# Performance work log

Measured on AMD Instinct MI355X. Metric: run time of the kernel, lower is better.

The kernel has to match this reference:

```python
import jax, jax.numpy as jnp
import numpy as np
import math

B, H, N, DH = 4, 8, 1024, 128
DPT = 4  # point feature dim (<=4 branch: squared-distance map only)

def setup_inputs() -> dict:
    key = jax.random.key(0)
    ks = jax.random.split(key, 10)
    q   = jax.random.normal(ks[0], (B, H, N, DH), jnp.float32)
    k   = jax.random.normal(ks[1], (B, H, N, DH), jnp.float32)
    v   = jax.random.normal(ks[2], (B, H, N, DH), jnp.float32)
    c   = jax.random.normal(ks[3], (B, H, N, 1), jnp.float32)
    d_q = jax.random.normal(ks[4], (B, N, DPT), jnp.float32)
    d_k = jax.random.normal(ks[5], (B, N, DPT), jnp.float32)
    # LazyLinear(1 -> nhead): per-head scalar weight + bias
    w_w = jax.random.normal(ks[6], (H,), jnp.float32) * 0.1
    b_w = jax.random.normal(ks[7], (H,), jnp.float32) * 0.1
    w_b = jax.random.normal(ks[8], (H,), jnp.float32) * 0.1
    b_b = jax.random.normal(ks[9], (H,), jnp.float32) * 0.1
    return {"q": q, "k": k, "v": v, "c": c, "d_q": d_q, "d_k": d_k,
            "w_w": w_w, "b_w": b_w, "w_b": w_b, "b_b": b_b}

def reference(q, k, v, c, d_q, d_k, w_w, b_w, w_b, b_b):
    dh = q.shape[-1]
    # pairwise squared distances on first 3 coords (torch: under no_grad)
    dq3 = d_q[:, :, :3]
    dk3 = d_k[:, :, :3]
    dist = jax.lax.stop_gradient(
        jnp.sum(dq3 ** 2, -1)[:, :, None]
        + jnp.sum(dk3 ** 2, -1)[:, None, :]
        - 2.0 * jnp.einsum('bnd,bmd->bnm', dq3, dk3))  # [B,N,M]
    db = dist[:, None, :, :]  # [B,1,N,M]
    wbc = lambda p: p[None, :, None, None]  # [1,H,1,1]
    # distmap_w = softplus(-(w*dist + b)); distmap_b = w*dist + b (identity acts)
    distmap_w = jax.nn.softplus(-(db * wbc(w_w) + wbc(b_w)))  # [B,H,N,M]
    distmap_b = db * wbc(w_b) + wbc(b_b)                      # [B,H,N,M]
    # scaled dot-product scores per head
    scores = jnp.einsum('bhnd,bhmd->bhnm', q, k) / math.sqrt(dh)
    scores = jax.nn.relu(scores * distmap_w + distmap_b)
    detr = (jnp.sum(scores, -1, keepdims=True)
            + jnp.sum(jax.nn.softplus(c), 2, keepdims=True) + 1e-9)
    scores = scores / detr
    out = jnp.einsum('bhnm,bhmd->bhnd', scores, v)
    return out, scores
```

## Files before the change

### kernel.cpp

```cpp
#include <hip/hip_runtime.h>


typedef __attribute__((ext_vector_type(8))) short short8;
typedef __attribute__((ext_vector_type(4))) float f32x4;

#define OUT_ELEMS 4194304ull
#define WS_K      0ull
#define WS_VT     8388608ull
#define WS_INVD   16777216ull
#define WS_CS     16908288ull

__device__ __forceinline__ unsigned short f2bf(float f) {
    unsigned u = __builtin_bit_cast(unsigned, f);
    u += 0x7FFFu + ((u >> 16) & 1u);
    return (unsigned short)(u >> 16);
}
__device__ __forceinline__ float softplus(float x) {
    return fmaxf(x, 0.f) + __logf(1.f + __expf(-fabsf(x)));
}

__global__ __launch_bounds__(256) void prep_k(const float* __restrict__ k, unsigned short* __restrict__ wsK) {
    int t = blockIdx.x * 256 + threadIdx.x;
    for (int u = t; u < 524288; u += 131072) {
        float4 a = reinterpret_cast<const float4*>(k)[u * 2];
        float4 b = reinterpret_cast<const float4*>(k)[u * 2 + 1];
        short8 o;
        o[0]=(short)f2bf(a.x); o[1]=(short)f2bf(a.y); o[2]=(short)f2bf(a.z); o[3]=(short)f2bf(a.w);
        o[4]=(short)f2bf(b.x); o[5]=(short)f2bf(b.y); o[6]=(short)f2bf(b.z); o[7]=(short)f2bf(b.w);
        reinterpret_cast<short8*>(wsK)[u] = o;
    }
}

__global__ __launch_bounds__(256) void prep_v(const float* __restrict__ v, unsigned short* __restrict__ wsVt) {
    __shared__ unsigned short sT[64 * 132];
    const int bh = blockIdx.x >> 4, m0 = (blockIdx.x & 15) * 64;
    const int tid = threadIdx.x;
    const float* src = v + ((size_t)bh * 1024 + m0) * 128;
    for (int i = tid; i < 2048; i += 256) {
        int row = i >> 5, c4 = i & 31;
        float4 t = reinterpret_cast<const float4*>(src)[i];
        unsigned long long pk = (unsigned long long)f2bf(t.x)
                              | ((unsigned long long)f2bf(t.y) << 16)
                              | ((unsigned long long)f2bf(t.z) << 32)
                              | ((unsigned long long)f2bf(t.w) << 48);
        *reinterpret_cast<unsigned long long*>(&sT[row * 132 + c4 * 4]) = pk;
    }
    __syncthreads();
    for (int u = tid; u < 2048; u += 256) {
        int dh = u >> 4, ms = u & 15;
        unsigned long long pk = (unsigned long long)sT[(ms*4+0)*132 + dh]
                              | ((unsigned long long)sT[(ms*4+1)*132 + dh] << 16)
                              | ((unsigned long long)sT[(ms*4+2)*132 + dh] << 32)
                              | ((unsigned long long)sT[(ms*4+3)*132 + dh] << 48);
        *reinterpret_cast<unsigned long long*>(&wsVt[((size_t)bh * 128 + dh) * 1024 + m0 + ms * 4]) = pk;
    }
}

__global__ __launch_bounds__(256) void prep_c(const float* __restrict__ c, float* __restrict__ wsCs) {
    __shared__ float red[4];
    const int bh = blockIdx.x, tid = threadIdx.x;
    float p = 0.f;
    for (int i = tid; i < 1024; i += 256) p += softplus(c[(size_t)bh * 1024 + i]);
    p += __shfl_xor(p, 32, 64); p += __shfl_xor(p, 16, 64); p += __shfl_xor(p, 8, 64);
    p += __shfl_xor(p,  4, 64); p += __shfl_xor(p,  2, 64); p += __shfl_xor(p, 1, 64);
    if ((tid & 63) == 0) red[tid >> 6] = p;
    __syncthreads();
    if (tid == 0) wsCs[bh] = red[0] + red[1] + red[2] + red[3] + 1e-9f;
}

__global__ __launch_bounds__(512, 4) void sam_main(
    const float* __restrict__ q, const float* __restrict__ dqp, const float* __restrict__ dkp,
    const float* __restrict__ w_w, const float* __restrict__ b_w,
    const float* __restrict__ w_b, const float* __restrict__ b_b,
    const unsigned short* __restrict__ wsK, const unsigned short* __restrict__ wsVt,
    const float* __restrict__ wsCs, float* __restrict__ wsInvd,
    float* __restrict__ out)
{
    __shared__ __align__(16) unsigned short sKall[2 * 8704];
    __shared__ __align__(16) unsigned short sVtall[2 * 9216];
    __shared__ float sdkall[2 * 256];
    __shared__ float s_inv[64];

    const int bid  = blockIdx.x;
    const int bh   = bid & 31;
    const int n0   = (bid >> 5) * 64;
    const int b    = bh >> 3;
    const int h    = bh & 7;
    const int tid  = threadIdx.x;
    const int lane = tid & 63;
    const int wave = tid >> 6;
    const int g    = wave >> 2;
    const int wl   = wave & 3;
    const int w16  = wl * 16;
    const int tg   = tid & 255;
    const int l15  = lane & 15;
    const int quad = lane >> 4;

    const float ww = w_w[h], bw = b_w[h], wb = w_b[h], bb = b_b[h];
    const float SCALE = 0.08838834764831845f;

    {
        const float* qbase = q + ((size_t)bh * 1024 + n0) * 128;
        for (int i = tid; i < 2048; i += 512) {
            int row = i >> 5, c4 = i & 31;
            float4 t = reinterpret_cast<const float4*>(qbase)[i];
            unsigned long long pk = (unsigned long long)f2bf(t.x)
                                  | ((unsigned long long)f2bf(t.y) << 16)
                                  | ((unsigned long long)f2bf(t.z) << 32)
                                  | ((unsigned long long)f2bf(t.w) << 48);
            *reinterpret_cast<unsigned long long*>(&sKall[row * 136 + c4 * 4]) = pk;
        }
    }
    float qx[4], qy[4], qz[4], qs[4];
    #pragma unroll
    for (int r = 0; r < 4; r++) {
        int nl = w16 + quad * 4 + r;
        float4 d4 = reinterpret_cast<const float4*>(dqp)[(size_t)b * 1024 + n0 + nl];
        qx[r] = d4.x; qy[r] = d4.y; qz[r] = d4.z;
        qs[r] = d4.x*d4.x + d4.y*d4.y + d4.z*d4.z;
    }
    const float cs = wsCs[bh];
    __syncthreads();
    short8 afr[4];
    {
        const unsigned short* aq = &sKall[(w16 + l15) * 136];
        #pragma unroll
        for (int ks = 0; ks < 4; ks++)
            afr[ks] = *reinterpret_cast<const short8*>(aq + ks * 32 + quad * 8);
    }
    __syncthreads();

    f32x4 oacc[8];
    #pragma unroll
    for (int i = 0; i < 8; i++) oacc[i] = {0.f, 0.f, 0.f, 0.f};
    float rs[4] = {0.f, 0.f, 0.f, 0.f};
    float* scb = out + OUT_ELEMS + ((size_t)bh << 20);

    unsigned short* sKg  = sKall  + g * 8704;
    unsigned short* sVtg = sVtall + g * 9216;
    unsigned short* sP   = sKg + wl * 1152;
    float* sdkg = sdkall + g * 256;

    for (int t8 = 0; t8 < 8; t8++) {
        const int m0 = (t8 * 2 + g) * 64;
        for (int i = tg; i < 1024; i += 256) {
            int row = i >> 4, seg = i & 15;
            short8 d = *reinterpret_cast<const short8*>(wsK + ((size_t)bh * 1024 + m0 + row) * 128 + seg * 8);
            *reinterpret_cast<short8*>(&sKg[row * 136 + seg * 8]) = d;
        }
        for (int i = tg; i < 1024; i += 256) {
            int dh = i >> 3, seg = i & 7;
            short8 d = *reinterpret_cast<const short8*>(wsVt + ((size_t)bh * 128 + dh) * 1024 + m0 + seg * 8);
            *reinterpret_cast<short8*>(&sVtg[dh * 72 + seg * 8]) = d;
        }
        if (tg < 64) {
            float4 d4 = reinterpret_cast<const float4*>(dkp)[(size_t)b * 1024 + m0 + tg];
            sdkg[tg] = d4.x; sdkg[64 + tg] = d4.y; sdkg[128 + tg] = d4.z;
            sdkg[192 + tg] = d4.x*d4.x + d4.y*d4.y + d4.z*d4.z;
        }
        __syncthreads();

        f32x4 cacc[4];
        #pragma unroll
        for (int mf = 0; mf < 4; mf++) {
            cacc[mf] = {0.f, 0.f, 0.f, 0.f};
            const unsigned short* bq = &sKg[(mf * 16 + l15) * 136];
            #pragma unroll
            for (int ks = 0; ks < 4; ks++) {
                short8 bfr = *reinterpret_cast<const short8*>(bq + ks * 32 + quad * 8);
                cacc[mf] = __builtin_amdgcn_mfma_f32_16x16x32_bf16(afr[ks], bfr, cacc[mf], 0, 0, 0);
            }
        }
        __syncthreads();

        #pragma unroll
        for (int mf = 0; mf < 4; mf++) {
            const int mloc = mf * 16 + l15;
            const float kx = sdkg[mloc], ky = sdkg[64 + mloc], kz = sdkg[128 + mloc], ksq = sdkg[192 + mloc];
            #pragma unroll
            for (int r = 0; r < 4; r++) {
                float dist = qs[r] + ksq - 2.f * (qx[r]*kx + qy[r]*ky + qz[r]*kz);
                float aw = softplus(-(dist * ww + bw));
                float ab = dist * wb + bb;
                float val = fmaxf(cacc[mf][r] * SCALE * aw + ab, 0.f);
                rs[r] += val;
                sP[(quad * 4 + r) * 72 + mf * 16 + l15] = f2bf(val);
                scb[(size_t)(n0 + w16 + quad * 4 + r) * 1024 + m0 + mf * 16 + l15] = val;
            }
        }
        #pragma unroll
        for (int ks2 = 0; ks2 < 2; ks2++) {
            short8 pfr = *reinterpret_cast<const short8*>(&sP[l15 * 72 + ks2 * 32 + quad * 8]);
            #pragma unroll
            for (int df = 0; df < 8; df++) {
                short8 vfr = *reinterpret_cast<const short8*>(&sVtg[(df * 16 + l15) * 72 + ks2 * 32 + quad * 8]);
                oacc[df] = __builtin_amdgcn_mfma_f32_16x16x32_bf16(pfr, vfr, oacc[df], 0, 0, 0);
            }
        }
        __syncthreads();
    }

    #pragma unroll
    for (int r = 0; r < 4; r++) {
        float t = rs[r];
        t += __shfl_xor(t, 1, 64); t += __shfl_xor(t, 2, 64);
        t += __shfl_xor(t, 4, 64); t += __shfl_xor(t, 8, 64);
        if (l15 == 0) sdkall[g * 256 + w16 + quad * 4 + r] = t;
    }
    __syncthreads();
    if (tid < 64) {
        float iv = 1.f / (sdkall[tid] + sdkall[256 + tid] + cs);
        s_inv[tid] = iv;
        wsInvd[(size_t)bh * 1024 + n0 + tid] = iv;
    }
    __syncthreads();

    float* sO = reinterpret_cast<float*>(sKall) + wl * 2112;
    if (g == 1) {
        #pragma unroll
        for (int df = 0; df < 8; df++)
            #pragma unroll
            for (int r = 0; r < 4; r++)
                sO[(quad * 4 + r) * 132 + df * 16 + l15] = oacc[df][r];
    }
    __syncthreads();
    if (g == 0) {
        #pragma unroll
        for (int df = 0; df < 8; df++) {
            #pragma unroll
            for (int r = 0; r < 4; r++) {
                int row = w16 + quad * 4 + r;
                float o = (oacc[df][r] + sO[(quad * 4 + r) * 132 + df * 16 + l15]) * s_inv[row];
                out[((size_t)bh * 1024 + n0 + row) * 128 + df * 16 + l15] = o;
            }
        }
    }
}

__global__ __launch_bounds__(256) void scale_sc(float* __restrict__ scores, const float* __restrict__ wsInvd) {
    const int row = blockIdx.x;
    const float iv = wsInvd[row];
    float4* p = reinterpret_cast<float4*>(scores + (size_t)row * 1024);
    float4 t = p[threadIdx.x];
    t.x *= iv; t.y *= iv; t.z *= iv; t.w *= iv;
    p[threadIdx.x] = t;
}

extern "C" void kernel_launch(void* const* d_in, const int* in_sizes, int n_in,
                              void* d_out, int out_size, void* d_ws, size_t ws_size,
                              hipStream_t stream) {
    const float* q   = (const float*)d_in[0];
    const float* k   = (const float*)d_in[1];
    const float* v   = (const float*)d_in[2];
    const float* c   = (const float*)d_in[3];
    const float* dq  = (const float*)d_in[4];
    const float* dk  = (const float*)d_in[5];
    const float* w_w = (const float*)d_in[6];
    const float* b_w = (const float*)d_in[7];
    const float* w_b = (const float*)d_in[8];
    const float* b_b = (const float*)d_in[9];
    float* out = (float*)d_out;
    char* ws = (char*)d_ws;
    unsigned short* wsK  = (unsigned short*)(ws + WS_K);
    unsigned short* wsVt = (unsigned short*)(ws + WS_VT);
    float* wsInvd = (float*)(ws + WS_INVD);
    float* wsCs   = (float*)(ws + WS_CS);

    hipLaunchKernelGGL(prep_k, dim3(512), dim3(256), 0, stream, k, wsK);
    hipLaunchKernelGGL(prep_v, dim3(512), dim3(256), 0, stream, v, wsVt);
    hipLaunchKernelGGL(prep_c, dim3(32),  dim3(256), 0, stream, c, wsCs);
    hipLaunchKernelGGL(sam_main, dim3(512), dim3(512), 0, stream,
                       q, dq, dk, w_w, b_w, w_b, b_b, wsK, wsVt, wsCs, wsInvd, out);
    hipLaunchKernelGGL(scale_sc, dim3(32768), dim3(256), 0, stream, out + OUT_ELEMS, wsInvd);
}
```

Before: 288.7 us.

## Stage unnormalized scores as bf16 in workspace and merge prep kernels

Result: faster. 273.1 us (-5.4%).

```diff
diff --git a/kernel.cpp b/kernel.cpp
--- a/kernel.cpp
+++ b/kernel.cpp
@@ -7,65 +7,72 @@
 #define OUT_ELEMS 4194304ull
 #define WS_K      0ull
 #define WS_VT     8388608ull
-#define WS_INVD   16777216ull
-#define WS_CS     16908288ull
+#define WS_P      16777216ull
+#define WS_INVD   83886080ull
+#define WS_CS     84017152ull
 
 __device__ __forceinline__ unsigned short f2bf(float f) {
     unsigned u = __builtin_bit_cast(unsigned, f);
     u += 0x7FFFu + ((u >> 16) & 1u);
     return (unsigned short)(u >> 16);
 }
+__device__ __forceinline__ float bf2f(unsigned short s) {
+    unsigned u = ((unsigned)s) << 16;
+    return __builtin_bit_cast(float, u);
+}
 __device__ __forceinline__ float softplus(float x) {
     return fmaxf(x, 0.f) + __logf(1.f + __expf(-fabsf(x)));
 }
 
-__global__ __launch_bounds__(256) void prep_k(const float* __restrict__ k, unsigned short* __restrict__ wsK) {
-    int t = blockIdx.x * 256 + threadIdx.x;
-    for (int u = t; u < 524288; u += 131072) {
-        float4 a = reinterpret_cast<const float4*>(k)[u * 2];
-        float4 b = reinterpret_cast<const float4*>(k)[u * 2 + 1];
-        short8 o;
-        o[0]=(short)f2bf(a.x); o[1]=(short)f2bf(a.y); o[2]=(short)f2bf(a.z); o[3]=(short)f2bf(a.w);
-        o[4]=(short)f2bf(b.x); o[5]=(short)f2bf(b.y); o[6]=(short)f2bf(b.z); o[7]=(short)f2bf(b.w);
-        reinterpret_cast<short8*>(wsK)[u] = o;
-    }
-}
-
-__global__ __launch_bounds__(256) void prep_v(const float* __restrict__ v, unsigned short* __restrict__ wsVt) {
+__global__ __launch_bounds__(256) void prep_all(
+    const float* __restrict__ k, const float* __restrict__ v, const float* __restrict__ c,
+    unsigned short* __restrict__ wsK, unsigned short* __restrict__ wsVt, float* __restrict__ wsCs)
+{
     __shared__ unsigned short sT[64 * 132];
-    const int bh = blockIdx.x >> 4, m0 = (blockIdx.x & 15) * 64;
-    const int tid = threadIdx.x;
-    const float* src = v + ((size_t)bh * 1024 + m0) * 128;
-    for (int i = tid; i < 2048; i += 256) {
-        int row = i >> 5, c4 = i & 31;
-        float4 t = reinterpret_cast<const float4*>(src)[i];
-        unsigned long long pk = (unsigned long long)f2bf(t.x)
-                              | ((unsigned long long)f2bf(t.y) << 16)
-                              | ((unsigned long long)f2bf(t.z) << 32)
-                              | ((unsigned long long)f2bf(t.w) << 48);
-        *reinterpret_cast<unsigned long long*>(&sT[row * 132 + c4 * 4]) = pk;
-    }
-    __syncthreads();
-    for (int u = tid; u < 2048; u += 256) {
-        int dh = u >> 4, ms = u & 15;
-        unsigned long long pk = (unsigned long long)sT[(ms*4+0)*132 + dh]
-                              | ((unsigned long long)sT[(ms*4+1)*132 + dh] << 16)
-                              | ((unsigned long long)sT[(ms*4+2)*132 + dh] << 32)
-                              | ((unsigned long long)sT[(ms*4+3)*132 + dh] << 48);
-        *reinterpret_cast<unsigned long long*>(&wsVt[((size_t)bh * 128 + dh) * 1024 + m0 + ms * 4]) = pk;
-    }
-}
-
-__global__ __launch_bounds__(256) void prep_c(const float* __restrict__ c, float* __restrict__ wsCs) {
-    __shared__ float red[4];
-    const int bh = blockIdx.x, tid = threadIdx.x;
-    float p = 0.f;
-    for (int i = tid; i < 1024; i += 256) p += softplus(c[(size_t)bh * 1024 + i]);
-    p += __shfl_xor(p, 32, 64); p += __shfl_xor(p, 16, 64); p += __shfl_xor(p, 8, 64);
-    p += __shfl_xor(p,  4, 64); p += __shfl_xor(p,  2, 64); p += __shfl_xor(p, 1, 64);
-    if ((tid & 63) == 0) red[tid >> 6] = p;
-    __syncthreads();
-    if (tid == 0) wsCs[bh] = red[0] + red[1] + red[2] + red[3] + 1e-9f;
+    const int blk = blockIdx.x, tid = threadIdx.x;
+    if (blk < 512) {
+        int t = blk * 256 + tid;
+        for (int u = t; u < 524288; u += 131072) {
+            float4 a = reinterpret_cast<const float4*>(k)[u * 2];
+            float4 b = reinterpret_cast<const float4*>(k)[u * 2 + 1];
+            short8 o;
+            o[0]=(short)f2bf(a.x); o[1]=(short)f2bf(a.y); o[2]=(short)f2bf(a.z); o[3]=(short)f2bf(a.w);
+            o[4]=(short)f2bf(b.x); o[5]=(short)f2bf(b.y); o[6]=(short)f2bf(b.z); o[7]=(short)f2bf(b.w);
+            reinterpret_cast<short8*>(wsK)[u] = o;
+        }
+    } else if (blk < 1024) {
+        const int vb = blk - 512;
+        const int bh = vb >> 4, m0 = (vb & 15) * 64;
+        const float* src = v + ((size_t)bh * 1024 + m0) * 128;
+        for (int i = tid; i < 2048; i += 256) {
+            int row = i >> 5, c4 = i & 31;
+            float4 t = reinterpret_cast<const float4*>(src)[i];
+            unsigned long long pk = (unsigned long long)f2bf(t.x)
+                                  | ((unsigned long long)f2bf(t.y) << 16)
+                                  | ((unsigned long long)f2bf(t.z) << 32)
+                                  | ((unsigned long long)f2bf(t.w) << 48);
+            *reinterpret_cast<unsigned long long*>(&sT[row * 132 + c4 * 4]) = pk;
+        }
+        __syncthreads();
+        for (int u = tid; u < 2048; u += 256) {
+            int dh = u >> 4, ms = u & 15;
+            unsigned long long pk = (unsigned long long)sT[(ms*4+0)*132 + dh]
+                                  | ((unsigned long long)sT[(ms*4+1)*132 + dh] << 16)
+                                  | ((unsigned long long)sT[(ms*4+2)*132 + dh] << 32)
+                                  | ((unsigned long long)sT[(ms*4+3)*132 + dh] << 48);
+            *reinterpret_cast<unsigned long long*>(&wsVt[((size_t)bh * 128 + dh) * 1024 + m0 + ms * 4]) = pk;
+        }
+    } else {
+        __shared__ float red[4];
+        const int bh = blk - 1024;
+        float p = 0.f;
+        for (int i = tid; i < 1024; i += 256) p += softplus(c[(size_t)bh * 1024 + i]);
+        p += __shfl_xor(p, 32, 64); p += __shfl_xor(p, 16, 64); p += __shfl_xor(p, 8, 64);
+        p += __shfl_xor(p,  4, 64); p += __shfl_xor(p,  2, 64); p += __shfl_xor(p, 1, 64);
+        if ((tid & 63) == 0) red[tid >> 6] = p;
+        __syncthreads();
+        if (tid == 0) wsCs[bh] = red[0] + red[1] + red[2] + red[3] + 1e-9f;
+    }
 }
 
 __global__ __launch_bounds__(512, 4) void sam_main(
@@ -74,7 +81,7 @@
     const float* __restrict__ w_b, const float* __restrict__ b_b,
     const unsigned short* __restrict__ wsK, const unsigned short* __restrict__ wsVt,
     const float* __restrict__ wsCs, float* __restrict__ wsInvd,
-    float* __restrict__ out)
+    unsigned short* __restrict__ wsP, float* __restrict__ out)
 {
     __shared__ __align__(16) unsigned short sKall[2 * 8704];
     __shared__ __align__(16) unsigned short sVtall[2 * 9216];
@@ -134,7 +141,6 @@
     #pragma unroll
     for (int i = 0; i < 8; i++) oacc[i] = {0.f, 0.f, 0.f, 0.f};
     float rs[4] = {0.f, 0.f, 0.f, 0.f};
-    float* scb = out + OUT_ELEMS + ((size_t)bh << 20);
 
     unsigned short* sKg  = sKall  + g * 8704;
     unsigned short* sVtg = sVtall + g * 9216;
@@ -185,7 +191,6 @@
                 float val = fmaxf(cacc[mf][r] * SCALE * aw + ab, 0.f);
                 rs[r] += val;
                 sP[(quad * 4 + r) * 72 + mf * 16 + l15] = f2bf(val);
-                scb[(size_t)(n0 + w16 + quad * 4 + r) * 1024 + m0 + mf * 16 + l15] = val;
             }
         }
         #pragma unroll
@@ -195,6 +200,16 @@
             for (int df = 0; df < 8; df++) {
                 short8 vfr = *reinterpret_cast<const short8*>(&sVtg[(df * 16 + l15) * 72 + ks2 * 32 + quad * 8]);
                 oacc[df] = __builtin_amdgcn_mfma_f32_16x16x32_bf16(pfr, vfr, oacc[df], 0, 0, 0);
+            }
+        }
+        {
+            unsigned short* dst = wsP + ((size_t)bh * 1024 + n0 + w16) * 1024 + m0;
+            #pragma unroll
+            for (int half = 0; half < 2; half++) {
+                int u = half * 64 + lane;
+                int row = u >> 3, seg = u & 7;
+                short8 d = *reinterpret_cast<const short8*>(&sP[row * 72 + seg * 8]);
+                *reinterpret_cast<short8*>(dst + (size_t)row * 1024 + seg * 8) = d;
             }
         }
         __syncthreads();
@@ -237,13 +252,20 @@
     }
 }
 
-__global__ __launch_bounds__(256) void scale_sc(float* __restrict__ scores, const float* __restrict__ wsInvd) {
+__global__ __launch_bounds__(256) void rescale(
+    const unsigned short* __restrict__ wsP, const float* __restrict__ wsInvd,
+    float* __restrict__ scores)
+{
     const int row = blockIdx.x;
     const float iv = wsInvd[row];
-    float4* p = reinterpret_cast<float4*>(scores + (size_t)row * 1024);
-    float4 t = p[threadIdx.x];
-    t.x *= iv; t.y *= iv; t.z *= iv; t.w *= iv;
-    p[threadIdx.x] = t;
+    const unsigned long long d = *reinterpret_cast<const unsigned long long*>(
+        wsP + (size_t)row * 1024 + threadIdx.x * 4);
+    float4 o;
+    o.x = bf2f((unsigned short)(d       & 0xFFFF)) * iv;
+    o.y = bf2f((unsigned short)((d>>16) & 0xFFFF)) * iv;
+    o.z = bf2f((unsigned short)((d>>32) & 0xFFFF)) * iv;
+    o.w = bf2f((unsigned short)((d>>48) & 0xFFFF)) * iv;
+    reinterpret_cast<float4*>(scores + (size_t)row * 1024)[threadIdx.x] = o;
 }
 
 extern "C" void kernel_launch(void* const* d_in, const int* in_sizes, int n_in,
@@ -263,13 +285,12 @@
     char* ws = (char*)d_ws;
     unsigned short* wsK  = (unsigned short*)(ws + WS_K);
     unsigned short* wsVt = (unsigned short*)(ws + WS_VT);
+    unsigned short* wsP  = (unsigned short*)(ws + WS_P);
     float* wsInvd = (float*)(ws + WS_INVD);
     float* wsCs   = (float*)(ws + WS_CS);
 
-    hipLaunchKernelGGL(prep_k, dim3(512), dim3(256), 0, stream, k, wsK);
-    hipLaunchKernelGGL(prep_v, dim3(512), dim3(256), 0, stream, v, wsVt);
-    hipLaunchKernelGGL(prep_c, dim3(32),  dim3(256), 0, stream, c, wsCs);
+    hipLaunchKernelGGL(prep_all, dim3(1056), dim3(256), 0, stream, k, v, c, wsK, wsVt, wsCs);
     hipLaunchKernelGGL(sam_main, dim3(512), dim3(512), 0, stream,
-                       q, dq, dk, w_w, b_w, w_b, b_b, wsK, wsVt, wsCs, wsInvd, out);
-    hipLaunchKernelGGL(scale_sc, dim3(32768), dim3(256), 0, stream, out + OUT_ELEMS, wsInvd);
-}
+                       q, dq, dk, w_w, b_w, w_b, b_b, wsK, wsVt, wsCs, wsInvd, wsP, out);
+    hipLaunchKernelGGL(rescale, dim3(32768), dim3(256), 0, stream, wsP, wsInvd, out + OUT_ELEMS);
+}
```
